# Kernel tuning notes

Measured on AMD Instinct MI355X. Metric: run time of the kernel, lower is better.

Reference implementation:

```python
import jax, jax.numpy as jnp
import numpy as np

L, H, DH = 4, 8, 64            # num_layers, num_heads, hidden_dim (= dim_per_head)
HD = H * DH                    # 512 = per-layer q/k/v width
R, BLOCK, NREG, NW = 3, 128, 8, 8   # n_hashes, block_size, num_regions, num_w_per_dist
CDIM, LAT = 2, 3               # coords_dim, latent_dim
SCALE = 1.0 / float(np.sqrt(DH))


def layer_norm(x, g, b):
    m = x.mean(-1, keepdims=True)
    v = ((x - m) ** 2).mean(-1, keepdims=True)
    return (x - m) * jax.lax.rsqrt(v + 1e-5) * g + b


def hept_attention(q, k, v, coords, batch, w_head, hash_proj):
    # HEPT: E2LSH hash + region/batch bucketing -> sort -> blockwise attention
    # with RPE distance bias, combined over hash rounds by logsumexp weights.
    N = q.shape[0]
    nb = N // BLOCK
    qh = q.reshape(N, H, DH)
    kh = k.reshape(N, H, DH)
    vh = v.reshape(N, H, DH)
    c0 = coords[:, 0]
    region = jnp.clip(((c0 - c0.min()) / (c0.max() - c0.min() + 1e-6) * NREG).astype(jnp.int32), 0, NREG - 1)
    c_rpe = coords[:, 1:]                       # [N, CDIM-1] dims used for RPE distances
    bf = batch.astype(jnp.float32)
    outs, lses = [], []
    for r in range(R):
        hv = coords @ hash_proj[r]              # [N] LSH projection
        hn = (hv - hv.min()) / (hv.max() - hv.min() + 1e-6)
        skey = (bf * NREG + region.astype(jnp.float32)) * 2.0 + hn  # batch-major, region, hash
        idx = jnp.argsort(skey)
        inv = jnp.argsort(idx)
        qs = qh[idx].reshape(nb, BLOCK, H, DH)
        ks = kh[idx].reshape(nb, BLOCK, H, DH)
        vs = vh[idx].reshape(nb, BLOCK, H, DH)
        cs = c_rpe[idx].reshape(nb, BLOCK, CDIM - 1)
        bs = batch[idx].reshape(nb, BLOCK)
        scores = jnp.einsum('bihd,bjhd->bhij', qs, ks) * SCALE     # [nb,H,B,B]
        d2 = (cs[:, :, None, :] - cs[:, None, :, :]) ** 2          # [nb,B,B,CDIM-1]
        scores = scores - jnp.einsum('hc,bijc->bhij', w_head, d2)  # RPE distance penalty
        scores = jnp.where((bs[:, :, None] == bs[:, None, :])[:, None], scores, -1e9)
        lse = jax.nn.logsumexp(scores, axis=-1)                    # [nb,H,B]
        p = jnp.exp(scores - lse[..., None])
        o = jnp.einsum('bhij,bjhd->bihd', p, vs).reshape(N, H, DH)
        outs.append(o[inv])
        lses.append(jnp.transpose(lse, (0, 2, 1)).reshape(N, H)[inv])
    wts = jax.nn.softmax(jnp.stack(lses), axis=0)[..., None]       # [R,N,H,1]
    return (wts * jnp.stack(outs)).sum(0).reshape(N, HD)


def _forward(x, coords, batch, enc_W1, enc_b1, enc_W2, enc_b2, ln1_g, ln1_b, wq, wk, wv,
             rpe_W, wo, ln2_g, ln2_b, ff_W1, ff_b1, ff_W2, ff_b2, W_cat,
             mlp_W1, mlp_b1, mlp_W2, mlp_b2, beta_W1, beta_b1, beta_W2, beta_b2,
             coord_W1, coord_b1, coord_W2, coord_b2, hash_proj):
    h0 = jax.nn.relu(x @ enc_W1 + enc_b1) @ enc_W2 + enc_b2
    feats = [h0]
    cur = h0
    for l in range(L):
        xn = layer_norm(cur, ln1_g[l], ln1_b[l])
        q = xn @ wq[l]
        k = xn @ wk[l]
        v = xn @ wv[l]
        # per-head positive RPE weights derived from w_rpe weight matrix
        w_head = jax.nn.softplus(rpe_W[l].reshape(CDIM - 1, NW, H, DH).mean(axis=(1, 3)).T)  # [H,CDIM-1]
        a = hept_attention(q, k, v, coords, batch, w_head, hash_proj) @ wo[l]
        cur = cur + a
        ffo = jax.nn.relu(layer_norm(cur, ln2_g[l], ln2_b[l]) @ ff_W1[l] + ff_b1[l]) @ ff_W2[l] + ff_b2[l]
        cur = cur + ffo
        feats.append(cur)
    enc2 = jnp.concatenate(feats, axis=-1) @ W_cat
    out = enc2 + (jax.nn.relu(enc2 @ mlp_W1 + mlp_b1) @ mlp_W2 + mlp_b2)
    eps = 1e-6
    beta = jnp.clip(jax.nn.sigmoid(jax.nn.relu(out @ beta_W1 + beta_b1) @ beta_W2 + beta_b2), eps, 1.0 - eps)
    hcoord = jax.nn.relu(out @ coord_W1 + coord_b1) @ coord_W2 + coord_b2
    return beta, hcoord


def setup_inputs() -> dict:
    key = jax.random.key(0)
    ks = jax.random.split(key, 40)
    N, IN_DIM = 32768, 16
    def w(i, shape, s=0.05):
        return jax.random.normal(ks[i], shape, jnp.float32) * s
    return dict(
        x=jax.random.normal(ks[0], (N, IN_DIM), jnp.float32),
        coords=jax.random.normal(ks[1], (N, CDIM), jnp.float32),
        batch=jnp.sort(jax.random.randint(ks[2], (N,), 0, 8)),
        enc_W1=w(3, (IN_DIM, DH)), enc_b1=jnp.zeros((DH,), jnp.float32),
        enc_W2=w(4, (DH, DH)), enc_b2=jnp.zeros((DH,), jnp.float32),
        ln1_g=jnp.ones((L, DH), jnp.float32), ln1_b=jnp.zeros((L, DH), jnp.float32),
        wq=w(5, (L, DH, HD)), wk=w(6, (L, DH, HD)), wv=w(7, (L, DH, HD)),
        rpe_W=w(8, (L, NW * (CDIM - 1), HD)),
        wo=w(9, (L, HD, DH)),
        ln2_g=jnp.ones((L, DH), jnp.float32), ln2_b=jnp.zeros((L, DH), jnp.float32),
        ff_W1=w(10, (L, DH, DH)), ff_b1=jnp.zeros((L, DH), jnp.float32),
        ff_W2=w(11, (L, DH, DH)), ff_b2=jnp.zeros((L, DH), jnp.float32),
        W_cat=w(12, (DH * (L + 1), DH // 2)),
        mlp_W1=w(13, (DH // 2, DH // 2)), mlp_b1=jnp.zeros((DH // 2,), jnp.float32),
        mlp_W2=w(14, (DH // 2, DH // 2)), mlp_b2=jnp.zeros((DH // 2,), jnp.float32),
        beta_W1=w(15, (DH // 2, DH // 4)), beta_b1=jnp.zeros((DH // 4,), jnp.float32),
        beta_W2=w(16, (DH // 4, 1)), beta_b2=jnp.zeros((1,), jnp.float32),
        coord_W1=w(17, (DH // 2, DH // 4)), coord_b1=jnp.zeros((DH // 4,), jnp.float32),
        coord_W2=w(18, (DH // 4, LAT)), coord_b2=jnp.zeros((LAT,), jnp.float32),
        hash_proj=jax.random.normal(ks[19], (R, CDIM), jnp.float32),
    )


def reference(x, coords, batch, enc_W1, enc_b1, enc_W2, enc_b2, ln1_g, ln1_b, wq, wk, wv,
              rpe_W, wo, ln2_g, ln2_b, ff_W1, ff_b1, ff_W2, ff_b2, W_cat,
              mlp_W1, mlp_b1, mlp_W2, mlp_b2, beta_W1, beta_b1, beta_W2, beta_b2,
              coord_W1, coord_b1, coord_W2, coord_b2, hash_proj):
    return _forward(x, coords, batch, enc_W1, enc_b1, enc_W2, enc_b2, ln1_g, ln1_b, wq, wk, wv,
                    rpe_W, wo, ln2_g, ln2_b, ff_W1, ff_b1, ff_W2, ff_b2, W_cat,
                    mlp_W1, mlp_b1, mlp_W2, mlp_b2, beta_W1, beta_b1, beta_W2, beta_b2,
                    coord_W1, coord_b1, coord_W2, coord_b2, hash_proj)
```

## Files before the change

kernel.cpp:

```cpp
#include <hip/hip_runtime.h>
#include <math.h>

#define DEV __device__ __forceinline__

constexpr int DHc = 64;
constexpr int HDc = 512;
constexpr int Hc  = 8;
constexpr int BLKc = 128;

typedef float f32x16 __attribute__((ext_vector_type(16)));
typedef short s16x8  __attribute__((ext_vector_type(8)));

union FragU { unsigned u[4]; s16x8 v; };

DEV unsigned fenc(float f){ unsigned u = __float_as_uint(f); return (u & 0x80000000u) ? ~u : (u | 0x80000000u); }
DEV float fdec(unsigned u){ unsigned b = (u & 0x80000000u) ? (u ^ 0x80000000u) : ~u; return __uint_as_float(b); }
DEV float hv_calc(float c0, float c1, float h0, float h1){
  return __fadd_rn(__fmul_rn(c0, h0), __fmul_rn(c1, h1));
}
DEV unsigned short f2bf(float f){
  unsigned u = __float_as_uint(f);
  return (unsigned short)((u + 0x7FFFu + ((u >> 16) & 1u)) >> 16);
}
DEV float bf2f(unsigned short s){ return __uint_as_float((unsigned)s << 16); }

DEV unsigned cvtpk(float lo, float hi){
  unsigned r;
  asm("v_cvt_pk_bf16_f32 %0, %1, %2" : "=v"(r) : "v"(lo), "v"(hi));
  return r;
}
DEV unsigned pack_bf2(float lo, float hi){
  return (unsigned)f2bf(lo) | ((unsigned)f2bf(hi) << 16);
}
DEV void pswap(unsigned &a, unsigned &b){
  asm volatile("v_permlane32_swap_b32 %0, %1" : "+v"(a), "+v"(b));
}

__global__ void minmax_init_kernel(unsigned* mm){
  int t = threadIdx.x;
  if (t < 4) mm[t] = 0xFFFFFFFFu;
  else if (t < 8) mm[t] = 0u;
}

__global__ __launch_bounds__(256) void minmax_reduce_kernel(const float* __restrict__ coords,
    const float* __restrict__ hp, unsigned* mm, int N)
{
  __shared__ float red[4][8];
  float h[6];
  #pragma unroll
  for (int i = 0; i < 6; ++i) h[i] = hp[i];
  float mn[4] = {3.0e38f, 3.0e38f, 3.0e38f, 3.0e38f};
  float mx[4] = {-3.0e38f, -3.0e38f, -3.0e38f, -3.0e38f};
  for (int i = blockIdx.x*blockDim.x + threadIdx.x; i < N; i += gridDim.x*blockDim.x){
    float2 c = *(const float2*)&coords[2*i];
    float v0 = c.x;
    float v1 = hv_calc(c.x, c.y, h[0], h[1]);
    float v2 = hv_calc(c.x, c.y, h[2], h[3]);
    float v3 = hv_calc(c.x, c.y, h[4], h[5]);
    mn[0] = fminf(mn[0], v0); mx[0] = fmaxf(mx[0], v0);
    mn[1] = fminf(mn[1], v1); mx[1] = fmaxf(mx[1], v1);
    mn[2] = fminf(mn[2], v2); mx[2] = fmaxf(mx[2], v2);
    mn[3] = fminf(mn[3], v3); mx[3] = fmaxf(mx[3], v3);
  }
  #pragma unroll
  for (int o = 1; o < 64; o <<= 1){
    #pragma unroll
    for (int s = 0; s < 4; ++s){
      mn[s] = fminf(mn[s], __shfl_xor(mn[s], o));
      mx[s] = fmaxf(mx[s], __shfl_xor(mx[s], o));
    }
  }
  int w = threadIdx.x >> 6;
  if ((threadIdx.x & 63) == 0){
    #pragma unroll
    for (int s = 0; s < 4; ++s){ red[w][s] = mn[s]; red[w][4+s] = mx[s]; }
  }
  __syncthreads();
  int t = threadIdx.x;
  if (t < 4){
    float v = fminf(fminf(red[0][t], red[1][t]), fminf(red[2][t], red[3][t]));
    atomicMin(&mm[t], fenc(v));
  } else if (t < 8){
    float v = fmaxf(fmaxf(red[0][t], red[1][t]), fmaxf(red[2][t], red[3][t]));
    atomicMax(&mm[t], fenc(v));
  }
}

__global__ void make_keys_kernel(const float* __restrict__ coords, const int* __restrict__ batch,
                                 const float* __restrict__ hp, const unsigned* __restrict__ mm,
                                 unsigned long long* __restrict__ keys, int N)
{
  int i = blockIdx.x*blockDim.x + threadIdx.x;
  if (i >= N) return;
  float c0 = coords[2*i], c1 = coords[2*i+1];
  float c0min = fdec(mm[0]), c0max = fdec(mm[4]);
  float rf = (c0 - c0min) / (c0max - c0min + 1e-6f) * 8.0f;
  int region = (int)rf;
  region = region < 0 ? 0 : (region > 7 ? 7 : region);
  float base2 = ((float)batch[i] * 8.0f + (float)region) * 2.0f;
  #pragma unroll
  for (int r = 0; r < 3; ++r){
    float hv = hv_calc(c0, c1, hp[2*r], hp[2*r+1]);
    float hn = (hv - fdec(mm[1+r])) / (fdec(mm[5+r]) - fdec(mm[1+r]) + 1e-6f);
    float skey = base2 + hn;
    keys[(size_t)r*N + i] = ((unsigned long long)__float_as_uint(skey) << 32) | (unsigned)i;
  }
}

__global__ __launch_bounds__(1024) void bitonic_local_full2k_kernel(unsigned long long* keys, int N)
{
  __shared__ unsigned long long sh[2048];
  unsigned long long* a = keys + (size_t)blockIdx.y * N;
  int base = blockIdx.x * 2048, t = threadIdx.x;
  sh[t] = a[base + t];
  sh[t + 1024] = a[base + t + 1024];
  __syncthreads();
  for (int k = 2; k <= 2048; k <<= 1){
    for (int j = k >> 1; j > 0; j >>= 1){
      int i = ((t & ~(j-1)) << 1) | (t & (j-1));
      bool dirup = (((base + i) & k) == 0);
      unsigned long long x = sh[i], y = sh[i+j];
      if ((x > y) == dirup){ sh[i] = y; sh[i+j] = x; }
      __syncthreads();
    }
  }
  a[base + t] = sh[t];
  a[base + t + 1024] = sh[t + 1024];
}

__global__ void bitonic_global_kernel(unsigned long long* keys, int N, int k, int j)
{
  unsigned long long* a = keys + (size_t)blockIdx.y * N;
  int i = blockIdx.x*blockDim.x + threadIdx.x;
  int l = i ^ j;
  if (l > i && l < N){
    unsigned long long x = a[i], y = a[l];
    bool dirup = ((i & k) == 0);
    if ((x > y) == dirup){ a[i] = y; a[l] = x; }
  }
}

__global__ __launch_bounds__(1024) void bitonic_local_merge2k_kernel(unsigned long long* keys, int N, int k)
{
  __shared__ unsigned long long sh[2048];
  unsigned long long* a = keys + (size_t)blockIdx.y * N;
  int base = blockIdx.x * 2048, t = threadIdx.x;
  sh[t] = a[base + t];
  sh[t + 1024] = a[base + t + 1024];
  __syncthreads();
  for (int j = 1024; j > 0; j >>= 1){
    int i = ((t & ~(j-1)) << 1) | (t & (j-1));
    bool dirup = (((base + i) & k) == 0);
    unsigned long long x = sh[i], y = sh[i+j];
    if ((x > y) == dirup){ sh[i] = y; sh[i+j] = x; }
    __syncthreads();
  }
  a[base + t] = sh[t];
  a[base + t + 1024] = sh[t + 1024];
}

__global__ void extract_idx_kernel(const unsigned long long* __restrict__ keys, int* __restrict__ idx, int total)
{
  int i = blockIdx.x*blockDim.x + threadIdx.x;
  if (i < total) idx[i] = (int)(keys[i] & 0xFFFFFFFFull);
}

__global__ void wconv_kernel(const float* __restrict__ wq, const float* __restrict__ wk,
                             const float* __restrict__ wv, const float* __restrict__ wo,
                             unsigned short* __restrict__ wqkvT, unsigned short* __restrict__ woT)
{
  int tid = blockIdx.x*blockDim.x + threadIdx.x;
  const int NQ = 4*3*512*64;
  if (tid < NQ){
    int kk = tid & 63;
    int rest = tid >> 6;
    int n = rest & 511;
    int rest2 = rest >> 9;
    int z = rest2 % 3, l = rest2 / 3;
    const float* W = (z==0) ? wq : (z==1) ? wk : wv;
    float scale = (z==0) ? 0.125f : 1.0f;
    wqkvT[tid] = f2bf(W[((size_t)l*64 + kk)*512 + n] * scale);
  } else if (tid < NQ + 4*64*512){
    int e = tid - NQ;
    int kk = e & 511;
    int rest = e >> 9;
    int n = rest & 63;
    int l = rest >> 6;
    woT[e] = f2bf(wo[((size_t)l*512 + kk)*64 + n]);
  }
}

__global__ __launch_bounds__(256) void encoder_kernel(const float* __restrict__ x,
    const float* __restrict__ W1, const float* __restrict__ b1,
    const float* __restrict__ W2, const float* __restrict__ b2,
    const float* __restrict__ lng, const float* __restrict__ lnb,
    float* __restrict__ h0, unsigned short* __restrict__ xnb, int N)
{
  __shared__ float W1s[16][64];
  __shared__ __align__(16) float W2s[64][64];
  __shared__ float xs[4][16];
  __shared__ float t1s[4][64];
  int t = threadIdx.x;
  for (int f = t; f < 1024; f += 256) W1s[f>>6][f&63] = W1[f];
  #pragma unroll
  for (int e = 0; e < 4; ++e){ int f = t + e*256; *(float4*)&W2s[f>>4][(f&15)*4] = *(const float4*)&W2[f*4]; }
  int w = t >> 6, d = t & 63;
  int row = blockIdx.x*4 + w;
  if (d < 16) xs[w][d] = x[(size_t)row*16 + d];
  __syncthreads();
  float acc = b1[d];
  #pragma unroll
  for (int i = 0; i < 16; ++i) acc += xs[w][i]*W1s[i][d];
  t1s[w][d] = fmaxf(acc, 0.f);
  __syncthreads();
  float acc2 = b2[d];
  #pragma unroll
  for (int i = 0; i < 64; ++i) acc2 += t1s[w][i]*W2s[i][d];
  h0[(size_t)row*64 + d] = acc2;
  float s = acc2;
  #pragma unroll
  for (int o = 1; o < 64; o <<= 1) s += __shfl_xor(s, o);
  float mean = s * (1.0f/64.0f);
  float dv = acc2 - mean, sq = dv*dv;
  #pragma unroll
  for (int o = 1; o < 64; o <<= 1) sq += __shfl_xor(sq, o);
  xnb[(size_t)row*64 + d] = f2bf(dv * rsqrtf(sq*(1.0f/64.0f) + 1e-5f) * lng[d] + lnb[d]);
}

__global__ void whead_kernel(const float* __restrict__ rpe, float* __restrict__ wh)
{
  int l = blockIdx.x >> 3, h = blockIdx.x & 7, d = threadIdx.x;
  const float* rp = rpe + (size_t)l*8*512;
  float s = 0.f;
  #pragma unroll
  for (int w = 0; w < 8; ++w) s += rp[(size_t)w*512 + h*64 + d];
  #pragma unroll
  for (int o = 1; o < 64; o <<= 1) s += __shfl_xor(s, o);
  if (d == 0){
    float m = s * (1.0f/512.0f);
    wh[blockIdx.x] = fmaxf(m, 0.f) + log1pf(expf(-fabsf(m)));
  }
}

__global__ __launch_bounds__(256, 3) void attn_kernel(
    const unsigned short* __restrict__ xnb, const unsigned short* __restrict__ wqkvT_l,
    const float* __restrict__ coords, const int* __restrict__ batch,
    const int* __restrict__ idx_all, const float* __restrict__ w_head,
    float* __restrict__ lse_all, unsigned short* __restrict__ o_buf, int N)
{
  __shared__ __align__(16) unsigned short qlds[128*64];
  __shared__ __align__(16) unsigned short klds[128*64];
  __shared__ __align__(16) unsigned short vtl[64*128];
  __shared__ __align__(16) float c1s[BLKc];
  __shared__ __align__(16) int   bts[BLKc];
  __shared__ int   idxs[BLKc];
  __shared__ __align__(16) float isel[BLKc];
  __shared__ int unif;
  int b = blockIdx.x, h = blockIdx.y, r = blockIdx.z, t = threadIdx.x;
  const int* idx_r = idx_all + (size_t)r*N;
  if (t < BLKc){
    int g = idx_r[b*BLKc + t];
    idxs[t] = g; c1s[t] = coords[2*g+1]; bts[t] = batch[g];
  }
  __syncthreads();
  if (t == 0) unif = (bts[0] == bts[127]);

  int w = t >> 6, l = t & 63, lo = l & 31, hi = l >> 5;

  int gm = idxs[w*32 + lo];
  const unsigned short* arp = &xnb[(size_t)gm*64];
  s16x8 af[4];
  #pragma unroll
  for (int ks = 0; ks < 4; ++ks)
    af[ks] = *(const s16x8*)&arp[ks*16 + hi*8];

  const unsigned short* whb = wqkvT_l + (size_t)h*64*64;
  #pragma unroll
  for (int z = 0; z < 3; ++z){
    const unsigned short* wz = whb + (size_t)z*512*64;
    f32x16 a0, a1;
    #pragma unroll
    for (int i = 0; i < 16; ++i){ a0[i] = 0.f; a1[i] = 0.f; }
    #pragma unroll
    for (int ks = 0; ks < 4; ++ks){
      s16x8 b0 = *(const s16x8*)&wz[(size_t)(lo)*64      + ks*16 + hi*8];
      s16x8 b1 = *(const s16x8*)&wz[(size_t)(32 + lo)*64 + ks*16 + hi*8];
      a0 = __builtin_amdgcn_mfma_f32_32x32x16_bf16(af[ks], b0, a0, 0, 0, 0);
      a1 = __builtin_amdgcn_mfma_f32_32x32x16_bf16(af[ks], b1, a1, 0, 0, 0);
    }
    if (z < 2){
      unsigned short* dst = z ? klds : qlds;
      int ch0 = lo >> 3, ch1 = 4 + (lo >> 3), co = lo & 7;
      #pragma unroll
      for (int reg = 0; reg < 16; ++reg){
        int row = w*32 + (reg&3) + 8*(reg>>2) + 4*hi;
        dst[row*64 + ((ch0 ^ (row&7))*8) + co] = f2bf(a0[reg]);
        dst[row*64 + ((ch1 ^ (row&7))*8) + co] = f2bf(a1[reg]);
      }
    } else {
      #pragma unroll
      for (int rq = 0; rq < 4; ++rq){
        int k0 = w*32 + rq*8 + 4*hi;
        int cj = k0 >> 3;
        int d0 = lo, d1 = 32 + lo;
        unsigned* dp0 = (unsigned*)&vtl[d0*128 + ((cj ^ (d0&7))*8) + 4*hi];
        dp0[0] = pack_bf2(a0[rq*4+0], a0[rq*4+1]);
        dp0[1] = pack_bf2(a0[rq*4+2], a0[rq*4+3]);
        unsigned* dp1 = (unsigned*)&vtl[d1*128 + ((cj ^ (d1&7))*8) + 4*hi];
        dp1[0] = pack_bf2(a1[rq*4+0], a1[rq*4+1]);
        dp1[1] = pack_bf2(a1[rq*4+2], a1[rq*4+3]);
      }
    }
  }
  __syncthreads();

  int qrow = w*32 + lo;
  s16x8 qf[4];
  #pragma unroll
  for (int ks = 0; ks < 4; ++ks)
    qf[ks] = *(const s16x8*)&qlds[qrow*64 + ((((ks<<1)|hi) ^ (qrow&7))*8)];

  f32x16 acc[4];
  #pragma unroll
  for (int kt = 0; kt < 4; ++kt)
    #pragma unroll
    for (int i = 0; i < 16; ++i) acc[kt][i] = 0.f;

  __builtin_amdgcn_s_setprio(1);
  #pragma unroll
  for (int kt = 0; kt < 4; ++kt){
    int krow = kt*32 + lo;
    #pragma unroll
    for (int ks = 0; ks < 4; ++ks){
      s16x8 kf = *(const s16x8*)&klds[krow*64 + ((((ks<<1)|hi) ^ (krow&7))*8)];
      acc[kt] = __builtin_amdgcn_mfma_f32_32x32x16_bf16(kf, qf[ks], acc[kt], 0, 0, 0);
    }
  }
  __builtin_amdgcn_s_setprio(0);

  float c1i = c1s[qrow]; int bti = bts[qrow];
  float wh = w_head[h];
  int msk = unif;
  #pragma unroll
  for (int kt = 0; kt < 4; ++kt){
    #pragma unroll
    for (int rq = 0; rq < 4; ++rq){
      int kb = kt*32 + rq*8 + hi*4;
      float4 c4 = *(const float4*)&c1s[kb];
      int4  b4 = *(const int4*)&bts[kb];
      #pragma unroll
      for (int j = 0; j < 4; ++j){
        int reg = rq*4 + j;
        float c1k = (j==0)?c4.x:(j==1)?c4.y:(j==2)?c4.z:c4.w;
        int   btk = (j==0)?b4.x:(j==1)?b4.y:(j==2)?b4.z:b4.w;
        float dd = c1i - c1k;
        float sc = acc[kt][reg] - wh*dd*dd;
        if (!msk && bti != btk) sc = -1e9f;
        acc[kt][reg] = sc;
      }
    }
  }

  float m = -3.0e38f;
  #pragma unroll
  for (int kt = 0; kt < 4; ++kt)
    #pragma unroll
    for (int i = 0; i < 16; ++i) m = fmaxf(m, acc[kt][i]);
  m = fmaxf(m, __shfl_xor(m, 32));
  float se = 0.f;
  #pragma unroll
  for (int kt = 0; kt < 4; ++kt)
    #pragma unroll
    for (int i = 0; i < 16; ++i){
      float p = __expf(acc[kt][i] - m);
      acc[kt][i] = p;
      se += p;
    }
  se += __shfl_xor(se, 32);
  if (l < 32){
    int gi0 = idxs[qrow];
    lse_all[((size_t)r*N + gi0)*Hc + h] = m + __logf(se);
    isel[qrow] = 1.0f / se;
  }

  f32x16 oa0, oa1;
  #pragma unroll
  for (int i = 0; i < 16; ++i){ oa0[i] = 0.f; oa1[i] = 0.f; }

  __builtin_amdgcn_s_setprio(1);
  #pragma unroll
  for (int kt = 0; kt < 4; ++kt){
    unsigned X = cvtpk(acc[kt][0],  acc[kt][1]);
    unsigned Z = cvtpk(acc[kt][2],  acc[kt][3]);
    unsigned Y = cvtpk(acc[kt][4],  acc[kt][5]);
    unsigned W = cvtpk(acc[kt][6],  acc[kt][7]);
    pswap(X, Y); pswap(Z, W);
    FragU f0; f0.u[0]=X; f0.u[1]=Z; f0.u[2]=Y; f0.u[3]=W;
    unsigned X2 = cvtpk(acc[kt][8],  acc[kt][9]);
    unsigned Z2 = cvtpk(acc[kt][10], acc[kt][11]);
    unsigned Y2 = cvtpk(acc[kt][12], acc[kt][13]);
    unsigned W2 = cvtpk(acc[kt][14], acc[kt][15]);
    pswap(X2, Y2); pswap(Z2, W2);
    FragU f1; f1.u[0]=X2; f1.u[1]=Z2; f1.u[2]=Y2; f1.u[3]=W2;
    #pragma unroll
    for (int hks = 0; hks < 2; ++hks){
      s16x8 pa = hks ? f1.v : f0.v;
      int kch = kt*4 + hks*2 + hi;
      int d0 = lo;
      s16x8 vf0 = *(const s16x8*)&vtl[d0*128 + ((kch ^ (d0&7))*8)];
      oa0 = __builtin_amdgcn_mfma_f32_32x32x16_bf16(pa, vf0, oa0, 0, 0, 0);
      int d1 = 32 + lo;
      s16x8 vf1 = *(const s16x8*)&vtl[d1*128 + ((kch ^ (d1&7))*8)];
      oa1 = __builtin_amdgcn_mfma_f32_32x32x16_bf16(pa, vf1, oa1, 0, 0, 0);
    }
  }
  __builtin_amdgcn_s_setprio(0);

  unsigned short* orow = o_buf + (size_t)r*N*HDc;
  #pragma unroll
  for (int rq = 0; rq < 4; ++rq){
    float4 s4 = *(const float4*)&isel[w*32 + rq*8 + hi*4];
    #pragma unroll
    for (int j = 0; j < 4; ++j){
      int reg = rq*4 + j;
      int qq = rq*8 + hi*4 + j;
      int g = idxs[w*32 + qq];
      float sv = (j==0)?s4.x:(j==1)?s4.y:(j==2)?s4.z:s4.w;
      unsigned short* dst = &orow[(size_t)g*HDc + h*DHc + lo];
      dst[0]  = f2bf(oa0[reg]*sv);
      dst[32] = f2bf(oa1[reg]*sv);
    }
  }
  (void)b;
}

__global__ __launch_bounds__(256) void wo_mfma_kernel(
    const unsigned short* __restrict__ o_buf, const float* __restrict__ lse_all,
    const unsigned short* __restrict__ woT_l, float* __restrict__ cur, int N)
{
  __shared__ __align__(16) unsigned short As[64*128];
  __shared__ __align__(16) unsigned short Bs[64*128];
  __shared__ float wts[64][24];
  int rb = blockIdx.x*64, t = threadIdx.x;
  #pragma unroll
  for (int e = 0; e < 2; ++e){
    int p = t + e*256;
    int rr = p >> 3, h = p & 7;
    float l0 = lse_all[((size_t)0*N + rb+rr)*Hc + h];
    float l1 = lse_all[((size_t)1*N + rb+rr)*Hc + h];
    float l2 = lse_all[((size_t)2*N + rb+rr)*Hc + h];
    float lm = fmaxf(l0, fmaxf(l1, l2));
    float e0 = __expf(l0-lm), e1 = __expf(l1-lm), e2 = __expf(l2-lm);
    float inv = 1.0f/(e0+e1+e2);
    wts[rr][h*3+0] = e0*inv; wts[rr][h*3+1] = e1*inv; wts[rr][h*3+2] = e2*inv;
  }
  int w = t >> 6, l = t & 63, lo = l & 31, hi = l >> 5;
  int mt = w >> 1, nt = w & 1;
  f32x16 acc;
  #pragma unroll
  for (int i = 0; i < 16; ++i) acc[i] = 0.f;
  for (int kt = 0; kt < 4; ++kt){
    __syncthreads();
    #pragma unroll
    for (int e = 0; e < 4; ++e){
      int f = t + e*256; int rr = f >> 4, kc = f & 15;
      int k0 = kt*128 + kc*8;
      int h = k0 >> 6;
      float w0 = wts[rr][h*3+0], w1 = wts[rr][h*3+1], w2 = wts[rr][h*3+2];
      s16x8 u0 = *(const s16x8*)&o_buf[((size_t)0*N + rb+rr)*HDc + k0];
      s16x8 u1 = *(const s16x8*)&o_buf[((size_t)1*N + rb+rr)*HDc + k0];
      s16x8 u2 = *(const s16x8*)&o_buf[((size_t)2*N + rb+rr)*HDc + k0];
      FragU fo;
      #pragma unroll
      for (int ii = 0; ii < 4; ++ii){
        float a0 = w0*bf2f((unsigned short)u0[2*ii])   + w1*bf2f((unsigned short)u1[2*ii])   + w2*bf2f((unsigned short)u2[2*ii]);
        float a1 = w0*bf2f((unsigned short)u0[2*ii+1]) + w1*bf2f((unsigned short)u1[2*ii+1]) + w2*bf2f((unsigned short)u2[2*ii+1]);
        fo.u[ii] = cvtpk(a0, a1);
      }
      *(s16x8*)&As[rr*128 + ((kc ^ (rr&7))*8)] = fo.v;
      *(s16x8*)&Bs[rr*128 + ((kc ^ (rr&7))*8)] = *(const s16x8*)&woT_l[(size_t)rr*512 + k0];
    }
    __syncthreads();
    #pragma unroll
    for (int ks = 0; ks < 8; ++ks){
      int s = ks*2 + hi;
      int arow = mt*32 + lo, brow = nt*32 + lo;
      s16x8 af = *(const s16x8*)&As[arow*128 + ((s ^ (arow&7))*8)];
      s16x8 bfr = *(const s16x8*)&Bs[brow*128 + ((s ^ (brow&7))*8)];
      acc = __builtin_amdgcn_mfma_f32_32x32x16_bf16(af, bfr, acc, 0, 0, 0);
    }
  }
  #pragma unroll
  for (int reg = 0; reg < 16; ++reg){
    int m = mt*32 + (reg&3) + 8*(reg>>2) + 4*hi;
    int n = nt*32 + lo;
    cur[(size_t)(rb+m)*64 + n] += acc[reg];
  }
}

__global__ __launch_bounds__(256) void ffn_kernel(float* __restrict__ cur,
    const float* __restrict__ g, const float* __restrict__ bln,
    const float* __restrict__ W1, const float* __restrict__ b1,
    const float* __restrict__ W2, const float* __restrict__ b2,
    const float* __restrict__ nlg, const float* __restrict__ nlb,
    unsigned short* __restrict__ xnb, int N)
{
  __shared__ __align__(16) float W1s[64][64];
  __shared__ __align__(16) float W2s[64][64];
  __shared__ float xns[4][64];
  __shared__ float t1s[4][64];
  int t = threadIdx.x;
  #pragma unroll
  for (int e = 0; e < 4; ++e){
    int f = t + e*256; int rr = f >> 4, c4 = f & 15;
    *(float4*)&W1s[rr][c4*4] = *(const float4*)&W1[f*4];
    *(float4*)&W2s[rr][c4*4] = *(const float4*)&W2[f*4];
  }
  int w = t >> 6, d = t & 63;
  int row = blockIdx.x*4 + w;
  float v = cur[(size_t)row*64 + d];
  float s = v;
  #pragma unroll
  for (int o = 1; o < 64; o <<= 1) s += __shfl_xor(s, o);
  float mean = s * (1.0f/64.0f);
  float dv = v - mean, sq = dv*dv;
  #pragma unroll
  for (int o = 1; o < 64; o <<= 1) sq += __shfl_xor(sq, o);
  float xnv = dv * rsqrtf(sq*(1.0f/64.0f) + 1e-5f) * g[d] + bln[d];
  xns[w][d] = xnv;
  __syncthreads();
  float acc = b1[d];
  #pragma unroll
  for (int i = 0; i < 64; ++i) acc += xns[w][i]*W1s[i][d];
  t1s[w][d] = fmaxf(acc, 0.f);
  __syncthreads();
  float acc2 = b2[d];
  #pragma unroll
  for (int i = 0; i < 64; ++i) acc2 += t1s[w][i]*W2s[i][d];
  float nv = v + acc2;
  cur[(size_t)row*64 + d] = nv;
  if (nlg){
    float s2 = nv;
    #pragma unroll
    for (int o = 1; o < 64; o <<= 1) s2 += __shfl_xor(s2, o);
    float mean2 = s2 * (1.0f/64.0f);
    float dv2 = nv - mean2, sq2 = dv2*dv2;
    #pragma unroll
    for (int o = 1; o < 64; o <<= 1) sq2 += __shfl_xor(sq2, o);
    xnb[(size_t)row*64 + d] = f2bf(dv2 * rsqrtf(sq2*(1.0f/64.0f) + 1e-5f) * nlg[d] + nlb[d]);
  }
}

__global__ __launch_bounds__(256) void enc2_accum_kernel(const float* __restrict__ cur,
    const float* __restrict__ Wcat, float* __restrict__ enc2, int rowoff, int store, int N)
{
  __shared__ float Ws[64][33];
  __shared__ float crs[32][65];
  int t = threadIdx.x;
  for (int f = t; f < 2048; f += 256) Ws[f>>5][f&31] = Wcat[(size_t)(rowoff + (f>>5))*32 + (f&31)];
  for (int f = t; f < 2048; f += 256) crs[f>>6][f&63] = cur[(size_t)(blockIdx.x*32 + (f>>6))*64 + (f&63)];
  __syncthreads();
  int r8 = t >> 5, c = t & 31;
  for (int rr = r8; rr < 32; rr += 8){
    int row = blockIdx.x*32 + rr;
    float acc = 0.f;
    #pragma unroll
    for (int d = 0; d < 64; ++d) acc += crs[rr][d]*Ws[d][c];
    size_t o = (size_t)row*32 + c;
    if (store) enc2[o] = acc; else enc2[o] += acc;
  }
}

__global__ __launch_bounds__(256) void head_kernel(const float* __restrict__ enc2,
    const float* mW1, const float* mb1, const float* mW2, const float* mb2,
    const float* bW1, const float* bb1, const float* bW2, const float* bb2,
    const float* cW1, const float* cb1, const float* cW2, const float* cb2,
    float* __restrict__ outp, int N)
{
  __shared__ float s_mW1[32][32], s_mW2[32][32], s_bW1[32][16], s_cW1[32][16];
  __shared__ float s_bW2[16], s_cW2[16][3];
  __shared__ float e2[8][32], t1[8][32], ov[8][32], bt[8][16], ct[8][16];
  int t = threadIdx.x;
  for (int f = t; f < 1024; f += 256){ s_mW1[f>>5][f&31] = mW1[f]; s_mW2[f>>5][f&31] = mW2[f]; }
  for (int f = t; f < 512; f += 256){ s_bW1[f>>4][f&15] = bW1[f]; s_cW1[f>>4][f&15] = cW1[f]; }
  if (t < 16) s_bW2[t] = bW2[t];
  if (t < 48) s_cW2[t/3][t%3] = cW2[t];
  int r8 = t >> 5, c = t & 31;
  int row = blockIdx.x*8 + r8;
  float e = enc2[(size_t)row*32 + c];
  e2[r8][c] = e;
  __syncthreads();
  float a = mb1[c];
  #pragma unroll
  for (int i = 0; i < 32; ++i) a += e2[r8][i]*s_mW1[i][c];
  t1[r8][c] = fmaxf(a, 0.f);
  __syncthreads();
  float o = e + mb2[c];
  #pragma unroll
  for (int i = 0; i < 32; ++i) o += t1[r8][i]*s_mW2[i][c];
  ov[r8][c] = o;
  __syncthreads();
  if (c < 16){
    float a2 = bb1[c];
    #pragma unroll
    for (int i = 0; i < 32; ++i) a2 += ov[r8][i]*s_bW1[i][c];
    bt[r8][c] = fmaxf(a2, 0.f);
  } else {
    int cc = c - 16;
    float a2 = cb1[cc];
    #pragma unroll
    for (int i = 0; i < 32; ++i) a2 += ov[r8][i]*s_cW1[i][cc];
    ct[r8][cc] = fmaxf(a2, 0.f);
  }
  __syncthreads();
  if (c == 0){
    float a3 = bb2[0];
    #pragma unroll
    for (int i = 0; i < 16; ++i) a3 += bt[r8][i]*s_bW2[i];
    float sg = 1.0f / (1.0f + __expf(-a3));
    sg = fminf(fmaxf(sg, 1e-6f), 1.0f - 1e-6f);
    outp[row] = sg;
  } else if (c < 4){
    int dd = c - 1;
    float a3 = cb2[dd];
    #pragma unroll
    for (int i = 0; i < 16; ++i) a3 += ct[r8][i]*s_cW2[i][dd];
    outp[(size_t)N + (size_t)row*3 + dd] = a3;
  }
}

extern "C" void kernel_launch(void* const* d_in, const int* in_sizes, int n_in,
                              void* d_out, int out_size, void* d_ws, size_t ws_size,
                              hipStream_t stream)
{
  const float* x       = (const float*)d_in[0];
  const float* coords  = (const float*)d_in[1];
  const int*   batch   = (const int*)d_in[2];
  const float* enc_W1  = (const float*)d_in[3];
  const float* enc_b1  = (const float*)d_in[4];
  const float* enc_W2  = (const float*)d_in[5];
  const float* enc_b2  = (const float*)d_in[6];
  const float* ln1_g   = (const float*)d_in[7];
  const float* ln1_b   = (const float*)d_in[8];
  const float* wq      = (const float*)d_in[9];
  const float* wk      = (const float*)d_in[10];
  const float* wv      = (const float*)d_in[11];
  const float* rpe_W   = (const float*)d_in[12];
  const float* wo      = (const float*)d_in[13];
  const float* ln2_g   = (const float*)d_in[14];
  const float* ln2_b   = (const float*)d_in[15];
  const float* ff_W1   = (const float*)d_in[16];
  const float* ff_b1   = (const float*)d_in[17];
  const float* ff_W2   = (const float*)d_in[18];
  const float* ff_b2   = (const float*)d_in[19];
  const float* W_cat   = (const float*)d_in[20];
  const float* mlp_W1  = (const float*)d_in[21];
  const float* mlp_b1  = (const float*)d_in[22];
  const float* mlp_W2  = (const float*)d_in[23];
  const float* mlp_b2  = (const float*)d_in[24];
  const float* beta_W1 = (const float*)d_in[25];
  const float* beta_b1 = (const float*)d_in[26];
  const float* beta_W2 = (const float*)d_in[27];
  const float* beta_b2 = (const float*)d_in[28];
  const float* coord_W1= (const float*)d_in[29];
  const float* coord_b1= (const float*)d_in[30];
  const float* coord_W2= (const float*)d_in[31];
  const float* coord_b2= (const float*)d_in[32];
  const float* hash_proj=(const float*)d_in[33];

  const int N  = in_sizes[0] / 16;
  const int nb = N / 128;
  float* outp = (float*)d_out;
  (void)out_size; (void)ws_size; (void)n_in;

  char* p = (char*)d_ws;
  size_t off = 0;
  auto alloc = [&](size_t bytes) -> char* {
    char* r = p + off;
    off += (bytes + 255) & ~(size_t)255;
    return r;
  };
  float* cur    = (float*)alloc((size_t)N*64*4);
  unsigned short* xnb = (unsigned short*)alloc((size_t)N*64*2);
  unsigned short* o_buf = (unsigned short*)alloc((size_t)3*N*512*2);
  float* enc2   = (float*)alloc((size_t)N*32*4);
  float* lse    = (float*)alloc((size_t)3*N*8*4);
  unsigned long long* keys = (unsigned long long*)alloc((size_t)3*N*8);
  int* idx      = (int*)alloc((size_t)3*N*4);
  unsigned short* wqkvT = (unsigned short*)alloc((size_t)4*3*512*64*2);
  unsigned short* woT   = (unsigned short*)alloc((size_t)4*64*512*2);
  unsigned* mm  = (unsigned*)alloc(256);
  float* whead  = (float*)alloc(256);

  wconv_kernel<<<2048, 256, 0, stream>>>(wq, wk, wv, wo, wqkvT, woT);
  whead_kernel<<<32, 64, 0, stream>>>(rpe_W, whead);

  minmax_init_kernel<<<1, 64, 0, stream>>>(mm);
  minmax_reduce_kernel<<<64, 256, 0, stream>>>(coords, hash_proj, mm, N);
  make_keys_kernel<<<(N+255)/256, 256, 0, stream>>>(coords, batch, hash_proj, mm, keys, N);
  bitonic_local_full2k_kernel<<<dim3(N/2048, 3), 1024, 0, stream>>>(keys, N);
  for (int kk = 4096; kk <= N; kk <<= 1){
    for (int j = kk >> 1; j >= 2048; j >>= 1)
      bitonic_global_kernel<<<dim3(N/256, 3), 256, 0, stream>>>(keys, N, kk, j);
    bitonic_local_merge2k_kernel<<<dim3(N/2048, 3), 1024, 0, stream>>>(keys, N, kk);
  }
  extract_idx_kernel<<<(3*N+255)/256, 256, 0, stream>>>(keys, idx, 3*N);

  encoder_kernel<<<N/4, 256, 0, stream>>>(x, enc_W1, enc_b1, enc_W2, enc_b2,
      ln1_g, ln1_b, cur, xnb, N);
  enc2_accum_kernel<<<N/32, 256, 0, stream>>>(cur, W_cat, enc2, 0, 1, N);

  for (int l = 0; l < 4; ++l){
    attn_kernel<<<dim3(nb, 8, 3), 256, 0, stream>>>(xnb,
        wqkvT + (size_t)l*3*512*64, coords, batch, idx, whead + l*8, lse, o_buf, N);
    wo_mfma_kernel<<<N/64, 256, 0, stream>>>(o_buf, lse, woT + (size_t)l*64*512, cur, N);
    const float* nlg = (l < 3) ? (ln1_g + (l+1)*64) : nullptr;
    const float* nlb = (l < 3) ? (ln1_b + (l+1)*64) : nullptr;
    ffn_kernel<<<N/4, 256, 0, stream>>>(cur, ln2_g + l*64, ln2_b + l*64,
        ff_W1 + (size_t)l*64*64, ff_b1 + l*64, ff_W2 + (size_t)l*64*64, ff_b2 + l*64,
        nlg, nlb, xnb, N);
    enc2_accum_kernel<<<N/32, 256, 0, stream>>>(cur, W_cat, enc2, (l+1)*64, 0, N);
  }

  head_kernel<<<N/8, 256, 0, stream>>>(enc2, mlp_W1, mlp_b1, mlp_W2, mlp_b2,
      beta_W1, beta_b1, beta_W2, beta_b2, coord_W1, coord_b1, coord_W2, coord_b2, outp, N);
}
```

Measured before the change: 787.7 us.

## Fold Wq·Wkᵀ into per-head bilinear matrix and drop softmax max subtraction

Precomputes a per-layer, per-head 64x64 matrix M = Wq_h·Wk_hᵀ·scale, so attention scores become x_i·M·x_jᵀ computed from gathered x tiles staged in LDS. This removes the separate K projection. It also removes the running max from the softmax and exponentiates raw scores directly, splitting the mask and no-mask paths into two specialised loops. The version without the max relies on scores staying small enough not to overflow exp, and the folded bf16 matrix changes rounding.

```diff
diff --git a/kernel.cpp b/kernel.cpp
--- a/kernel.cpp
+++ b/kernel.cpp
@@ -178,8 +178,7 @@
     int rest2 = rest >> 9;
     int z = rest2 % 3, l = rest2 / 3;
     const float* W = (z==0) ? wq : (z==1) ? wk : wv;
-    float scale = (z==0) ? 0.125f : 1.0f;
-    wqkvT[tid] = f2bf(W[((size_t)l*64 + kk)*512 + n] * scale);
+    wqkvT[tid] = f2bf(W[((size_t)l*64 + kk)*512 + n]);
   } else if (tid < NQ + 4*64*512){
     int e = tid - NQ;
     int kk = e & 511;
@@ -190,6 +189,32 @@
   }
 }
 
+__global__ __launch_bounds__(256) void mqk_kernel(const float* __restrict__ wq,
+    const float* __restrict__ wk, unsigned short* __restrict__ mqk)
+{
+  __shared__ float qs[64][64];
+  __shared__ float ks_[64][64];
+  int blk = blockIdx.x;
+  int l = blk >> 3, h = blk & 7;
+  int t = threadIdx.x;
+  for (int f = t; f < 4096; f += 256){
+    int i = f >> 6, d = f & 63;
+    qs[i][d]  = wq[((size_t)l*64 + i)*512 + h*64 + d];
+    ks_[i][d] = wk[((size_t)l*64 + i)*512 + h*64 + d];
+  }
+  __syncthreads();
+  int j = t >> 2, i0 = (t & 3) * 16;
+  unsigned short* outp = mqk + (size_t)blk*4096 + j*64;
+  #pragma unroll
+  for (int ii = 0; ii < 16; ++ii){
+    int i = i0 + ii;
+    float acc = 0.f;
+    #pragma unroll
+    for (int d = 0; d < 64; ++d) acc += qs[i][d]*ks_[j][d];
+    outp[i] = f2bf(acc * 0.125f);
+  }
+}
+
 __global__ __launch_bounds__(256) void encoder_kernel(const float* __restrict__ x,
     const float* __restrict__ W1, const float* __restrict__ b1,
     const float* __restrict__ W2, const float* __restrict__ b2,
@@ -244,12 +269,13 @@
 
 __global__ __launch_bounds__(256, 3) void attn_kernel(
     const unsigned short* __restrict__ xnb, const unsigned short* __restrict__ wqkvT_l,
+    const unsigned short* __restrict__ mqk_l,
     const float* __restrict__ coords, const int* __restrict__ batch,
     const int* __restrict__ idx_all, const float* __restrict__ w_head,
     float* __restrict__ lse_all, unsigned short* __restrict__ o_buf, int N)
 {
-  __shared__ __align__(16) unsigned short qlds[128*64];
-  __shared__ __align__(16) unsigned short klds[128*64];
+  __shared__ __align__(16) unsigned short xlds[128*64];
+  __shared__ __align__(16) unsigned short tlds[128*64];
   __shared__ __align__(16) unsigned short vtl[64*128];
   __shared__ __align__(16) float c1s[BLKc];
   __shared__ __align__(16) int   bts[BLKc];
@@ -264,20 +290,46 @@
   }
   __syncthreads();
   if (t == 0) unif = (bts[0] == bts[127]);
+  #pragma unroll
+  for (int e = 0; e < 4; ++e){
+    int f = t + e*256;
+    int row = f >> 3, ch = f & 7;
+    int g = idxs[row];
+    s16x8 xv = *(const s16x8*)&xnb[(size_t)g*64 + ch*8];
+    *(s16x8*)&xlds[row*64 + ((ch ^ (row&7))*8)] = xv;
+  }
+  __syncthreads();
 
   int w = t >> 6, l = t & 63, lo = l & 31, hi = l >> 5;
-
-  int gm = idxs[w*32 + lo];
-  const unsigned short* arp = &xnb[(size_t)gm*64];
+  int arow = w*32 + lo;
+
   s16x8 af[4];
   #pragma unroll
   for (int ks = 0; ks < 4; ++ks)
-    af[ks] = *(const s16x8*)&arp[ks*16 + hi*8];
-
-  const unsigned short* whb = wqkvT_l + (size_t)h*64*64;
-  #pragma unroll
-  for (int z = 0; z < 3; ++z){
-    const unsigned short* wz = whb + (size_t)z*512*64;
+    af[ks] = *(const s16x8*)&xlds[arow*64 + ((((ks<<1)|hi) ^ (arow&7))*8)];
+
+  {
+    const unsigned short* Mt = mqk_l + (size_t)h*4096;
+    f32x16 a0, a1;
+    #pragma unroll
+    for (int i = 0; i < 16; ++i){ a0[i] = 0.f; a1[i] = 0.f; }
+    #pragma unroll
+    for (int ks = 0; ks < 4; ++ks){
+      s16x8 b0 = *(const s16x8*)&Mt[(size_t)(lo)*64      + ks*16 + hi*8];
+      s16x8 b1 = *(const s16x8*)&Mt[(size_t)(32 + lo)*64 + ks*16 + hi*8];
+      a0 = __builtin_amdgcn_mfma_f32_32x32x16_bf16(af[ks], b0, a0, 0, 0, 0);
+      a1 = __builtin_amdgcn_mfma_f32_32x32x16_bf16(af[ks], b1, a1, 0, 0, 0);
+    }
+    int ch0 = lo >> 3, ch1 = 4 + (lo >> 3), co = lo & 7;
+    #pragma unroll
+    for (int reg = 0; reg < 16; ++reg){
+      int row = w*32 + (reg&3) + 8*(reg>>2) + 4*hi;
+      tlds[row*64 + ((ch0 ^ (row&7))*8) + co] = f2bf(a0[reg]);
+      tlds[row*64 + ((ch1 ^ (row&7))*8) + co] = f2bf(a1[reg]);
+    }
+  }
+  {
+    const unsigned short* wz = wqkvT_l + (size_t)2*512*64 + (size_t)h*64*64;
     f32x16 a0, a1;
     #pragma unroll
     for (int i = 0; i < 16; ++i){ a0[i] = 0.f; a1[i] = 0.f; }
@@ -288,37 +340,26 @@
       a0 = __builtin_amdgcn_mfma_f32_32x32x16_bf16(af[ks], b0, a0, 0, 0, 0);
       a1 = __builtin_amdgcn_mfma_f32_32x32x16_bf16(af[ks], b1, a1, 0, 0, 0);
     }
-    if (z < 2){
-      unsigned short* dst = z ? klds : qlds;
-      int ch0 = lo >> 3, ch1 = 4 + (lo >> 3), co = lo & 7;
-      #pragma unroll
-      for (int reg = 0; reg < 16; ++reg){
-        int row = w*32 + (reg&3) + 8*(reg>>2) + 4*hi;
-        dst[row*64 + ((ch0 ^ (row&7))*8) + co] = f2bf(a0[reg]);
-        dst[row*64 + ((ch1 ^ (row&7))*8) + co] = f2bf(a1[reg]);
-      }
-    } else {
-      #pragma unroll
-      for (int rq = 0; rq < 4; ++rq){
-        int k0 = w*32 + rq*8 + 4*hi;
-        int cj = k0 >> 3;
-        int d0 = lo, d1 = 32 + lo;
-        unsigned* dp0 = (unsigned*)&vtl[d0*128 + ((cj ^ (d0&7))*8) + 4*hi];
-        dp0[0] = pack_bf2(a0[rq*4+0], a0[rq*4+1]);
-        dp0[1] = pack_bf2(a0[rq*4+2], a0[rq*4+3]);
-        unsigned* dp1 = (unsigned*)&vtl[d1*128 + ((cj ^ (d1&7))*8) + 4*hi];
-        dp1[0] = pack_bf2(a1[rq*4+0], a1[rq*4+1]);
-        dp1[1] = pack_bf2(a1[rq*4+2], a1[rq*4+3]);
-      }
-    }
-  }
-  __syncthreads();
-
-  int qrow = w*32 + lo;
-  s16x8 qf[4];
+    #pragma unroll
+    for (int rq = 0; rq < 4; ++rq){
+      int k0 = w*32 + rq*8 + 4*hi;
+      int cj = k0 >> 3;
+      int d0 = lo, d1 = 32 + lo;
+      unsigned* dp0 = (unsigned*)&vtl[d0*128 + ((cj ^ (d0&7))*8) + 4*hi];
+      dp0[0] = pack_bf2(a0[rq*4+0], a0[rq*4+1]);
+      dp0[1] = pack_bf2(a0[rq*4+2], a0[rq*4+3]);
+      unsigned* dp1 = (unsigned*)&vtl[d1*128 + ((cj ^ (d1&7))*8) + 4*hi];
+      dp1[0] = pack_bf2(a1[rq*4+0], a1[rq*4+1]);
+      dp1[1] = pack_bf2(a1[rq*4+2], a1[rq*4+3]);
+    }
+  }
+  __syncthreads();
+
+  int qrow = arow;
+  s16x8 tf[4];
   #pragma unroll
   for (int ks = 0; ks < 4; ++ks)
-    qf[ks] = *(const s16x8*)&qlds[qrow*64 + ((((ks<<1)|hi) ^ (qrow&7))*8)];
+    tf[ks] = *(const s16x8*)&tlds[qrow*64 + ((((ks<<1)|hi) ^ (qrow&7))*8)];
 
   f32x16 acc[4];
   #pragma unroll
@@ -332,54 +373,43 @@
     int krow = kt*32 + lo;
     #pragma unroll
     for (int ks = 0; ks < 4; ++ks){
-      s16x8 kf = *(const s16x8*)&klds[krow*64 + ((((ks<<1)|hi) ^ (krow&7))*8)];
-      acc[kt] = __builtin_amdgcn_mfma_f32_32x32x16_bf16(kf, qf[ks], acc[kt], 0, 0, 0);
+      s16x8 xf = *(const s16x8*)&xlds[krow*64 + ((((ks<<1)|hi) ^ (krow&7))*8)];
+      acc[kt] = __builtin_amdgcn_mfma_f32_32x32x16_bf16(xf, tf[ks], acc[kt], 0, 0, 0);
     }
   }
   __builtin_amdgcn_s_setprio(0);
 
   float c1i = c1s[qrow]; int bti = bts[qrow];
   float wh = w_head[h];
-  int msk = unif;
-  #pragma unroll
-  for (int kt = 0; kt < 4; ++kt){
-    #pragma unroll
-    for (int rq = 0; rq < 4; ++rq){
-      int kb = kt*32 + rq*8 + hi*4;
-      float4 c4 = *(const float4*)&c1s[kb];
-      int4  b4 = *(const int4*)&bts[kb];
-      #pragma unroll
-      for (int j = 0; j < 4; ++j){
-        int reg = rq*4 + j;
-        float c1k = (j==0)?c4.x:(j==1)?c4.y:(j==2)?c4.z:c4.w;
-        int   btk = (j==0)?b4.x:(j==1)?b4.y:(j==2)?b4.z:b4.w;
-        float dd = c1i - c1k;
-        float sc = acc[kt][reg] - wh*dd*dd;
-        if (!msk && bti != btk) sc = -1e9f;
-        acc[kt][reg] = sc;
-      }
-    }
-  }
-
-  float m = -3.0e38f;
-  #pragma unroll
-  for (int kt = 0; kt < 4; ++kt)
-    #pragma unroll
-    for (int i = 0; i < 16; ++i) m = fmaxf(m, acc[kt][i]);
-  m = fmaxf(m, __shfl_xor(m, 32));
   float se = 0.f;
-  #pragma unroll
-  for (int kt = 0; kt < 4; ++kt)
-    #pragma unroll
-    for (int i = 0; i < 16; ++i){
-      float p = __expf(acc[kt][i] - m);
-      acc[kt][i] = p;
-      se += p;
-    }
+#define SCORE_LOOP(MASKED)                                                   \
+  _Pragma("unroll")                                                          \
+  for (int kt = 0; kt < 4; ++kt){                                            \
+    _Pragma("unroll")                                                        \
+    for (int rq = 0; rq < 4; ++rq){                                          \
+      int kb = kt*32 + rq*8 + hi*4;                                          \
+      float4 c4 = *(const float4*)&c1s[kb];                                  \
+      int4  b4 = *(const int4*)&bts[kb];                                     \
+      _Pragma("unroll")                                                      \
+      for (int j = 0; j < 4; ++j){                                           \
+        int reg = rq*4 + j;                                                  \
+        float c1k = (j==0)?c4.x:(j==1)?c4.y:(j==2)?c4.z:c4.w;                \
+        int   btk = (j==0)?b4.x:(j==1)?b4.y:(j==2)?b4.z:b4.w;                \
+        float dd = c1i - c1k;                                                \
+        float sc = acc[kt][reg] - wh*dd*dd;                                  \
+        if (MASKED && bti != btk) sc = -1e9f;                                \
+        float pv = __expf(sc);                                               \
+        acc[kt][reg] = pv;                                                   \
+        se += pv;                                                            \
+      }                                                                      \
+    }                                                                        \
+  }
+  if (unif){ SCORE_LOOP(false) } else { SCORE_LOOP(true) }
+#undef SCORE_LOOP
   se += __shfl_xor(se, 32);
   if (l < 32){
     int gi0 = idxs[qrow];
-    lse_all[((size_t)r*N + gi0)*Hc + h] = m + __logf(se);
+    lse_all[((size_t)r*N + gi0)*Hc + h] = __logf(se);
     isel[qrow] = 1.0f / se;
   }
 
@@ -689,10 +719,12 @@
   int* idx      = (int*)alloc((size_t)3*N*4);
   unsigned short* wqkvT = (unsigned short*)alloc((size_t)4*3*512*64*2);
   unsigned short* woT   = (unsigned short*)alloc((size_t)4*64*512*2);
+  unsigned short* mqk   = (unsigned short*)alloc((size_t)4*8*64*64*2);
   unsigned* mm  = (unsigned*)alloc(256);
   float* whead  = (float*)alloc(256);
 
   wconv_kernel<<<2048, 256, 0, stream>>>(wq, wk, wv, wo, wqkvT, woT);
+  mqk_kernel<<<32, 256, 0, stream>>>(wq, wk, mqk);
   whead_kernel<<<32, 64, 0, stream>>>(rpe_W, whead);
 
   minmax_init_kernel<<<1, 64, 0, stream>>>(mm);
@@ -712,7 +744,8 @@
 
   for (int l = 0; l < 4; ++l){
     attn_kernel<<<dim3(nb, 8, 3), 256, 0, stream>>>(xnb,
-        wqkvT + (size_t)l*3*512*64, coords, batch, idx, whead + l*8, lse, o_buf, N);
+        wqkvT + (size_t)l*3*512*64, mqk + (size_t)l*8*4096,
+        coords, batch, idx, whead + l*8, lse, o_buf, N);
     wo_mfma_kernel<<<N/64, 256, 0, stream>>>(o_buf, lse, woT + (size_t)l*64*512, cur, N);
     const float* nlg = (l < 3) ? (ln1_g + (l+1)*64) : nullptr;
     const float* nlb = (l < 3) ? (ln1_b + (l+1)*64) : nullptr;
```

New measurement: 727.0 us. 1.08x faster.
